# Kernel optimization log

Measured on AMD Instinct MI355X. Metric: run time of the kernel, lower is better.

## Reference

```python
import jax, jax.numpy as jnp
import numpy as np

N, E, D, H, ED, L = 50000, 800000, 256, 8, 16, 6
C = D // H  # 32
NEG_SLOPE = 0.2
EPS = 1e-5


def setup_inputs() -> dict:
    key = jax.random.key(0)
    ks = jax.random.split(key, 16)
    f32 = jnp.float32
    return {
        "x": jax.random.normal(ks[0], (N, D), f32),
        "edge_index": jax.random.randint(ks[1], (2, E), 0, N, dtype=jnp.int64),
        "edge_attr": jax.random.normal(ks[2], (E, ED), f32),
        # shared GATConv params (single conv reused every step, as in the source)
        "W": jax.random.normal(ks[3], (D, D), f32) / np.sqrt(D),
        "att_src": jax.random.normal(ks[4], (H, C), f32) * 0.05,
        "att_dst": jax.random.normal(ks[5], (H, C), f32) * 0.05,
        "att_edge": jax.random.normal(ks[6], (H, C), f32) * 0.05,
        "W_edge": jax.random.normal(ks[7], (ED, D), f32) / np.sqrt(ED),
        "bias": jnp.zeros((D,), f32),
        # per-step FFN + LayerNorm params
        "ffn_w1": jax.random.normal(ks[8], (L, D, 4 * D), f32) / np.sqrt(D),
        "ffn_b1": jnp.zeros((L, 4 * D), f32),
        "ffn_w2": jax.random.normal(ks[9], (L, 4 * D, D), f32) / np.sqrt(4 * D),
        "ffn_b2": jnp.zeros((L, D), f32),
        "ln1_g": jnp.ones((L, D), f32),
        "ln1_b": jnp.zeros((L, D), f32),
        "ln2_g": jnp.ones((L, D), f32),
        "ln2_b": jnp.zeros((L, D), f32),
    }


def _layernorm(x, g, b):
    mu = jnp.mean(x, -1, keepdims=True)
    var = jnp.mean(jnp.square(x - mu), -1, keepdims=True)
    return (x - mu) * jax.lax.rsqrt(var + EPS) * g + b


def _gat_conv(m, edge_index, edge_attr, W, att_src, att_dst, att_edge, W_edge, bias):
    n = m.shape[0]
    x_proj = (m @ W).reshape(n, H, C)  # [N,H,C]
    # add self loops; edge_attr fill_value='mean' (PyG default): mean of incoming edge feats
    src0, dst0 = edge_index[0], edge_index[1]
    deg = jax.ops.segment_sum(jnp.ones_like(dst0, jnp.float32), dst0, n)
    ea_mean = jax.ops.segment_sum(edge_attr, dst0, n) / jnp.maximum(deg, 1.0)[:, None]
    loop = jnp.arange(n, dtype=src0.dtype)
    src = jnp.concatenate([src0, loop])
    dst = jnp.concatenate([dst0, loop])
    ea = jnp.concatenate([edge_attr, ea_mean], 0)
    e_proj = (ea @ W_edge).reshape(-1, H, C)  # [E+N,H,C]
    a_src = jnp.sum(x_proj * att_src, -1)  # [N,H]
    a_dst = jnp.sum(x_proj * att_dst, -1)  # [N,H]
    a_edge = jnp.sum(e_proj * att_edge, -1)  # [E+N,H]
    alpha = jax.nn.leaky_relu(a_src[src] + a_dst[dst] + a_edge, NEG_SLOPE)
    # softmax over edges grouped by destination node
    amax = jax.ops.segment_max(alpha, dst, n)  # every node has a self loop
    ex = jnp.exp(alpha - amax[dst])
    denom = jax.ops.segment_sum(ex, dst, n)
    attn = ex / denom[dst]  # [E+N,H]
    msg = x_proj[src] * attn[:, :, None]  # [E+N,H,C]
    out = jax.ops.segment_sum(msg, dst, n).reshape(n, H * C)
    return out + bias


def reference(x, edge_index, edge_attr, W, att_src, att_dst, att_edge, W_edge, bias,
              ffn_w1, ffn_b1, ffn_w2, ffn_b2, ln1_g, ln1_b, ln2_g, ln2_b):
    m = x
    for i in range(L):
        g = _gat_conv(m, edge_index, edge_attr, W, att_src, att_dst, att_edge, W_edge, bias)
        m = _layernorm(g + m, ln1_g[i], ln1_b[i])  # dropout is identity in eval
        h = jax.nn.relu(m @ ffn_w1[i] + ffn_b1[i]) @ ffn_w2[i] + ffn_b2[i]
        m = _layernorm(h + m, ln2_g[i], ln2_b[i])
    return m
```

## Files before the change

kernel.cpp:

```cpp
#include <hip/hip_runtime.h>
#include <math.h>

#define NN 50000
#define MP 50048
#define EE 800000
#define DD 256
#define HH 8
#define CC 32
#define EDIMK 16
#define LL 6
#define HID 1024
#define NEG 0.2f
#define LNEPS 1e-5f

using short8  = __attribute__((ext_vector_type(8))) short;
using floatx4 = __attribute__((ext_vector_type(4))) float;

static __device__ __forceinline__ float4 ld4(const float* p) {
    return *reinterpret_cast<const float4*>(p);
}
static __device__ __forceinline__ void st4(float* p, float4 v) {
    *reinterpret_cast<float4*>(p) = v;
}
static __device__ __forceinline__ float b2f(unsigned short u) {
    union { unsigned int i; float f; } v; v.i = ((unsigned int)u) << 16; return v.f;
}
static __device__ __forceinline__ unsigned short f2b(float f) {
    union { float f; unsigned int i; } v; v.f = f;
    unsigned int r = (v.i + 0x7fffu + ((v.i >> 16) & 1u)) >> 16;
    return (unsigned short)r;
}
static __device__ __forceinline__ void gload_lds16(const ushort* g, ushort* l) {
    __builtin_amdgcn_global_load_lds((const __attribute__((address_space(1))) void*)g,
                                     (__attribute__((address_space(3))) void*)l, 16, 0, 0);
}

__global__ void k_weh(const float* __restrict__ W_edge, const float* __restrict__ att_edge,
                      float* __restrict__ w_eh) {
    int t = threadIdx.x;
    if (t < EDIMK * HH) {
        int k = t >> 3, h = t & 7;
        float s = 0.f;
        for (int c = 0; c < CC; ++c) s += W_edge[k * DD + h * CC + c] * att_edge[h * CC + c];
        w_eh[t] = s;
    }
}

__global__ void k_edge_pre(const float* __restrict__ edge_attr, const int* __restrict__ ei,
                           const float* __restrict__ w_eh, float* __restrict__ a_edge,
                           int* __restrict__ deg) {
    __shared__ float sw[EDIMK * HH];
    if (threadIdx.x < EDIMK * HH) sw[threadIdx.x] = w_eh[threadIdx.x];
    __syncthreads();
    int e = blockIdx.x * blockDim.x + threadIdx.x;
    if (e >= EE) return;
    float ea[EDIMK];
#pragma unroll
    for (int k4 = 0; k4 < EDIMK; k4 += 4) {
        float4 v = ld4(edge_attr + (size_t)e * EDIMK + k4);
        ea[k4] = v.x; ea[k4 + 1] = v.y; ea[k4 + 2] = v.z; ea[k4 + 3] = v.w;
    }
#pragma unroll
    for (int h = 0; h < HH; ++h) {
        float s = 0.f;
#pragma unroll
        for (int k = 0; k < EDIMK; ++k) s += ea[k] * sw[k * HH + h];
        a_edge[(size_t)e * HH + h] = s;
    }
    atomicAdd(&deg[ei[EE + e]], 1);
}

__global__ void k_scan(const int* __restrict__ deg, int* __restrict__ rowptr) {
    __shared__ int sd[1024];
    __shared__ int soff;
    int tid = threadIdx.x;
    if (tid == 0) { soff = 0; rowptr[0] = 0; }
    __syncthreads();
    for (int base = 0; base < NN; base += 1024) {
        int v = (base + tid < NN) ? deg[base + tid] : 0;
        sd[tid] = v;
        __syncthreads();
        for (int s = 1; s < 1024; s <<= 1) {
            int t2 = (tid >= s) ? sd[tid - s] : 0;
            __syncthreads();
            sd[tid] += t2;
            __syncthreads();
        }
        int incl = sd[tid];
        int off = soff;
        if (base + tid < NN) rowptr[base + tid + 1] = off + incl;
        __syncthreads();
        if (tid == 1023) soff = off + incl;
        __syncthreads();
    }
}

__global__ void k_scatter(const int* __restrict__ ei, const int* __restrict__ rowptr,
                          int* __restrict__ cursor, int* __restrict__ s_src,
                          int* __restrict__ s_eid) {
    int e = blockIdx.x * blockDim.x + threadIdx.x;
    if (e >= EE) return;
    int dst = ei[EE + e];
    int p = rowptr[dst] + atomicAdd(&cursor[dst], 1);
    s_src[p] = ei[e];
    s_eid[p] = e;
}

__global__ void k_permute(const int* __restrict__ s_eid, const float* __restrict__ a_edge,
                          float* __restrict__ ae_csr) {
    size_t t = (size_t)blockIdx.x * blockDim.x + threadIdx.x;
    if (t >= (size_t)EE * HH) return;
    ae_csr[t] = a_edge[(size_t)s_eid[t >> 3] * HH + (t & 7)];
}

__global__ void k_selfmean(const int* __restrict__ rowptr, const float* __restrict__ ae_csr,
                           float* __restrict__ a_self) {
    int t = blockIdx.x * blockDim.x + threadIdx.x;
    if (t >= NN * HH) return;
    int n = t >> 3, h = t & 7;
    int k0 = rowptr[n], k1 = rowptr[n + 1];
    float s = 0.f;
    for (int k = k0; k < k1; ++k) s += ae_csr[(size_t)k * HH + h];
    int d = k1 - k0; if (d < 1) d = 1;
    a_self[t] = s / (float)d;
}

__global__ __launch_bounds__(1024) void k_trans(const float* __restrict__ src,
                                                ushort* __restrict__ dst, int K, int N) {
    __shared__ float s[32][33];
    const float* S = src + (size_t)blockIdx.z * K * N;
    ushort* D = dst + (size_t)blockIdx.z * K * N;
    int n0 = blockIdx.x * 32, k0 = blockIdx.y * 32;
    s[threadIdx.y][threadIdx.x] = S[(size_t)(k0 + threadIdx.y) * N + n0 + threadIdx.x];
    __syncthreads();
    D[(size_t)(n0 + threadIdx.y) * K + k0 + threadIdx.x] = f2b(s[threadIdx.x][threadIdx.y]);
}

__global__ void k_cvt(const float* __restrict__ x, float* __restrict__ m,
                      ushort* __restrict__ mb) {
    int t = blockIdx.x * blockDim.x + threadIdx.x;
    if (t >= NN * DD) return;
    float v = x[t];
    m[t] = v;
    mb[t] = f2b(v);
}

__global__ __launch_bounds__(256) void k_gemm_bf16(const ushort* __restrict__ A,
                                                   const ushort* __restrict__ Bt,
                                                   const float* __restrict__ bias,
                                                   void* __restrict__ Cout,
                                                   int Nc, int K, int mode) {
    __shared__ ushort As[128 * 32];
    __shared__ ushort Bs[128 * 32];
    int tid = threadIdx.x;
    int w = tid >> 6, lane = tid & 63;
    int tileM = blockIdx.y * 128, tileN = blockIdx.x * 128;
    int lrow = lane >> 2, slot = lane & 3;
    int rA0 = w * 16 + lrow, rA1 = (w + 4) * 16 + lrow;
    int cA0 = (slot - (rA0 >> 1)) & 3;
    int cA1 = (slot - (rA1 >> 1)) & 3;
    const ushort* gA0 = A + (size_t)(tileM + rA0) * K + cA0 * 8;
    const ushort* gA1 = A + (size_t)(tileM + rA1) * K + cA1 * 8;
    const ushort* gB0 = Bt + (size_t)(tileN + rA0) * K + cA0 * 8;
    const ushort* gB1 = Bt + (size_t)(tileN + rA1) * K + cA1 * 8;
    ushort* lA0 = As + w * 512;
    ushort* lA1 = As + (w + 4) * 512;
    ushort* lB0 = Bs + w * 512;
    ushort* lB1 = Bs + (w + 4) * 512;
    int wr = w >> 1, wc = w & 1;
    int fr = lane & 15, q = lane >> 4;
    int sf = (q + (fr >> 1)) & 3;
    const ushort* fA = As + (wr * 64 + fr) * 32 + sf * 8;
    const ushort* fB = Bs + (wc * 64 + fr) * 32 + sf * 8;
    floatx4 acc[4][4] = {};
    for (int k0 = 0; k0 < K; k0 += 32) {
        __syncthreads();
        gload_lds16(gA0 + k0, lA0);
        gload_lds16(gA1 + k0, lA1);
        gload_lds16(gB0 + k0, lB0);
        gload_lds16(gB1 + k0, lB1);
        __syncthreads();
        short8 af[4], bf[4];
#pragma unroll
        for (int i = 0; i < 4; ++i) af[i] = *(const short8*)(fA + i * 16 * 32);
#pragma unroll
        for (int j = 0; j < 4; ++j) bf[j] = *(const short8*)(fB + j * 16 * 32);
#pragma unroll
        for (int i = 0; i < 4; ++i)
#pragma unroll
            for (int j = 0; j < 4; ++j)
                acc[i][j] = __builtin_amdgcn_mfma_f32_16x16x32_bf16(af[i], bf[j], acc[i][j], 0, 0, 0);
    }
    int rbase = tileM + wr * 64 + q * 4;
    int cbase = tileN + wc * 64 + fr;
#pragma unroll
    for (int j = 0; j < 4; ++j) {
        int col = cbase + j * 16;
        float bb = (mode != 1) ? bias[col] : 0.f;
#pragma unroll
        for (int i = 0; i < 4; ++i) {
            int row = rbase + i * 16;
#pragma unroll
            for (int r = 0; r < 4; ++r) {
                float v = acc[i][j][r] + bb;
                if (mode == 2 && v < 0.f) v = 0.f;
                if (mode == 0)
                    ((float*)Cout)[(size_t)(row + r) * Nc + col] = v;
                else
                    ((ushort*)Cout)[(size_t)(row + r) * Nc + col] = f2b(v);
            }
        }
    }
}

__global__ void k_srcdst(const ushort* __restrict__ xb, const float* __restrict__ att_src,
                         const float* __restrict__ att_dst, float* __restrict__ a_src,
                         float* __restrict__ a_dst) {
    __shared__ float ss[DD], sd[DD];
    int tid = threadIdx.x;
    if (tid < DD) { ss[tid] = att_src[tid]; sd[tid] = att_dst[tid]; }
    __syncthreads();
    int t = blockIdx.x * blockDim.x + tid;
    if (t >= NN * HH) return;
    int n = t >> 3, h = t & 7;
    const ushort* xp = xb + (size_t)n * DD + h * CC;
    float s1 = 0.f, s2 = 0.f;
#pragma unroll
    for (int c = 0; c < CC; c += 4) {
        ushort4 u = *(const ushort4*)(xp + c);
        float vx = b2f(u.x), vy = b2f(u.y), vz = b2f(u.z), vw = b2f(u.w);
        int b = h * CC + c;
        s1 += vx * ss[b] + vy * ss[b + 1] + vz * ss[b + 2] + vw * ss[b + 3];
        s2 += vx * sd[b] + vy * sd[b + 1] + vz * sd[b + 2] + vw * sd[b + 3];
    }
    a_src[t] = s1;
    a_dst[t] = s2;
}

__global__ __launch_bounds__(256) void k_agg(const ushort* __restrict__ xb,
                                             const float* __restrict__ a_src,
                                             const float* __restrict__ a_dst,
                                             const float* __restrict__ a_self,
                                             const int* __restrict__ rowptr,
                                             const int* __restrict__ s_src,
                                             const float* __restrict__ ae_csr,
                                             const float* __restrict__ bias,
                                             const float* __restrict__ gma,
                                             const float* __restrict__ bta,
                                             float* __restrict__ m,
                                             ushort* __restrict__ mb) {
    int wid = (blockIdx.x * blockDim.x + threadIdx.x) >> 6;
    int lane = threadIdx.x & 63;
    if (wid >= NN) return;
    int n = wid, h = lane >> 3, c4 = lane * 4;
    float adn = a_dst[n * HH + h];
    float al0 = a_src[n * HH + h] + adn + a_self[n * HH + h];
    al0 = al0 > 0.f ? al0 : NEG * al0;
    float w0 = __expf(al0);
    ushort4 xs = *(const ushort4*)(xb + (size_t)n * DD + c4);
    float den = w0;
    float ax = w0 * b2f(xs.x), ay = w0 * b2f(xs.y);
    float az = w0 * b2f(xs.z), aw = w0 * b2f(xs.w);
    int k0 = rowptr[n], k1 = rowptr[n + 1];
    int sNext = (k0 < k1) ? s_src[k0] : 0;
    for (int k = k0; k < k1; ++k) {
        int s = sNext;
        if (k + 1 < k1) sNext = s_src[k + 1];
        float al = a_src[(size_t)s * HH + h] + adn + ae_csr[(size_t)k * HH + h];
        al = al > 0.f ? al : NEG * al;
        float wv = __expf(al);
        den += wv;
        ushort4 v = *(const ushort4*)(xb + (size_t)s * DD + c4);
        ax += wv * b2f(v.x); ay += wv * b2f(v.y);
        az += wv * b2f(v.z); aw += wv * b2f(v.w);
    }
    float inv = 1.f / den;
    size_t base = (size_t)n * DD + c4;
    float4 mr = ld4(m + base);
    float4 b4 = ld4(bias + c4);
    float gx = ax * inv + b4.x + mr.x;
    float gy = ay * inv + b4.y + mr.y;
    float gz = az * inv + b4.z + mr.z;
    float gw = aw * inv + b4.w + mr.w;
    float s = gx + gy + gz + gw;
    for (int off = 32; off; off >>= 1) s += __shfl_xor(s, off, 64);
    float mu = s * (1.0f / DD);
    float dx = gx - mu, dy = gy - mu, dz = gz - mu, dw = gw - mu;
    float qv = dx * dx + dy * dy + dz * dz + dw * dw;
    for (int off = 32; off; off >>= 1) qv += __shfl_xor(qv, off, 64);
    float rs = rsqrtf(qv * (1.0f / DD) + LNEPS);
    float4 g4 = ld4(gma + c4), bb = ld4(bta + c4);
    float4 o;
    o.x = dx * rs * g4.x + bb.x; o.y = dy * rs * g4.y + bb.y;
    o.z = dz * rs * g4.z + bb.z; o.w = dw * rs * g4.w + bb.w;
    st4(m + base, o);
    ushort4 ob;
    ob.x = f2b(o.x); ob.y = f2b(o.y); ob.z = f2b(o.z); ob.w = f2b(o.w);
    *reinterpret_cast<ushort4*>(mb + base) = ob;
}

__global__ __launch_bounds__(256) void k_addln2(const float* __restrict__ a,
                                                const float* __restrict__ gma,
                                                const float* __restrict__ bta,
                                                float* __restrict__ m,
                                                ushort* __restrict__ mb) {
    int wid = (blockIdx.x * blockDim.x + threadIdx.x) >> 6;
    int lane = threadIdx.x & 63;
    if (wid >= NN) return;
    size_t base = (size_t)wid * DD + lane * 4;
    float4 va = ld4(a + base), vb = ld4(m + base);
    float4 v;
    v.x = va.x + vb.x; v.y = va.y + vb.y; v.z = va.z + vb.z; v.w = va.w + vb.w;
    float s = v.x + v.y + v.z + v.w;
    for (int off = 32; off; off >>= 1) s += __shfl_xor(s, off, 64);
    float mu = s * (1.0f / DD);
    float4 d;
    d.x = v.x - mu; d.y = v.y - mu; d.z = v.z - mu; d.w = v.w - mu;
    float qv = d.x * d.x + d.y * d.y + d.z * d.z + d.w * d.w;
    for (int off = 32; off; off >>= 1) qv += __shfl_xor(qv, off, 64);
    float rs = rsqrtf(qv * (1.0f / DD) + LNEPS);
    float4 g4 = ld4(gma + lane * 4), b4 = ld4(bta + lane * 4);
    float4 o;
    o.x = d.x * rs * g4.x + b4.x; o.y = d.y * rs * g4.y + b4.y;
    o.z = d.z * rs * g4.z + b4.z; o.w = d.w * rs * g4.w + b4.w;
    st4(m + base, o);
    ushort4 ob;
    ob.x = f2b(o.x); ob.y = f2b(o.y); ob.z = f2b(o.z); ob.w = f2b(o.w);
    *reinterpret_cast<ushort4*>(mb + base) = ob;
}

extern "C" void kernel_launch(void* const* d_in, const int* in_sizes, int n_in,
                              void* d_out, int out_size, void* d_ws, size_t ws_size,
                              hipStream_t stream) {
    const float* x        = (const float*)d_in[0];
    const int*   ei       = (const int*)d_in[1];
    const float* edge_attr= (const float*)d_in[2];
    const float* W        = (const float*)d_in[3];
    const float* att_src  = (const float*)d_in[4];
    const float* att_dst  = (const float*)d_in[5];
    const float* att_edge = (const float*)d_in[6];
    const float* W_edge   = (const float*)d_in[7];
    const float* bias     = (const float*)d_in[8];
    const float* ffn_w1   = (const float*)d_in[9];
    const float* ffn_b1   = (const float*)d_in[10];
    const float* ffn_w2   = (const float*)d_in[11];
    const float* ffn_b2   = (const float*)d_in[12];
    const float* ln1_g    = (const float*)d_in[13];
    const float* ln1_b    = (const float*)d_in[14];
    const float* ln2_g    = (const float*)d_in[15];
    const float* ln2_b    = (const float*)d_in[16];
    float* m = (float*)d_out;

    char* wp = (char*)d_ws;
    auto alloc = [&](size_t bytes) -> char* {
        char* p = wp;
        wp += (bytes + 255) & ~(size_t)255;
        return p;
    };
    float*  a_edge = (float*)alloc((size_t)EE * HH * 4);
    float*  ae_csr = (float*)alloc((size_t)EE * HH * 4);
    float*  a_self = (float*)alloc((size_t)NN * HH * 4);
    float*  a_src  = (float*)alloc((size_t)NN * HH * 4);
    float*  a_dst  = (float*)alloc((size_t)NN * HH * 4);
    int*    deg    = (int*)alloc((size_t)NN * 4);
    int*    rowptr = (int*)alloc((size_t)(NN + 1) * 4);
    int*    cursor = (int*)alloc((size_t)NN * 4);
    int*    s_src  = (int*)alloc((size_t)EE * 4);
    int*    s_eid  = (int*)alloc((size_t)EE * 4);
    float*  w_eh   = (float*)alloc((size_t)EDIMK * HH * 4);
    ushort* Wt     = (ushort*)alloc((size_t)DD * DD * 2);
    ushort* w1t    = (ushort*)alloc((size_t)LL * DD * HID * 2);
    ushort* w2t    = (ushort*)alloc((size_t)LL * HID * DD * 2);
    ushort* xprojb = (ushort*)alloc((size_t)MP * DD * 2);
    ushort* m_b    = (ushort*)alloc((size_t)MP * DD * 2);
    float*  gbuf   = (float*)alloc((size_t)MP * DD * 4);
    size_t used = (size_t)(wp - (char*)d_ws);
    size_t avail = ws_size > used ? ws_size - used : 0;
    size_t maxrows = avail / ((size_t)HID * 2);
    int chunkP = (int)((maxrows / 128) * 128);
    if (chunkP < 128) chunkP = 128;
    if (chunkP > MP) chunkP = MP;
    ushort* h1b = (ushort*)wp;

    hipMemsetAsync(deg, 0, (size_t)NN * 4, stream);
    hipMemsetAsync(cursor, 0, (size_t)NN * 4, stream);

    k_weh<<<1, 128, 0, stream>>>(W_edge, att_edge, w_eh);
    k_edge_pre<<<(EE + 255) / 256, 256, 0, stream>>>(edge_attr, ei, w_eh, a_edge, deg);
    k_scan<<<1, 1024, 0, stream>>>(deg, rowptr);
    k_scatter<<<(EE + 255) / 256, 256, 0, stream>>>(ei, rowptr, cursor, s_src, s_eid);
    k_permute<<<(EE * HH + 255) / 256, 256, 0, stream>>>(s_eid, a_edge, ae_csr);
    k_selfmean<<<(NN * HH + 255) / 256, 256, 0, stream>>>(rowptr, ae_csr, a_self);
    k_trans<<<dim3(DD / 32, DD / 32, 1), dim3(32, 32), 0, stream>>>(W, Wt, DD, DD);
    k_trans<<<dim3(HID / 32, DD / 32, LL), dim3(32, 32), 0, stream>>>(ffn_w1, w1t, DD, HID);
    k_trans<<<dim3(DD / 32, HID / 32, LL), dim3(32, 32), 0, stream>>>(ffn_w2, w2t, HID, DD);
    k_cvt<<<(NN * DD + 255) / 256, 256, 0, stream>>>(x, m, m_b);

    for (int i = 0; i < LL; ++i) {
        k_gemm_bf16<<<dim3(DD / 128, MP / 128), 256, 0, stream>>>(m_b, Wt, nullptr, xprojb, DD, DD, 1);
        k_srcdst<<<(NN * HH + 255) / 256, 256, 0, stream>>>(xprojb, att_src, att_dst, a_src, a_dst);
        k_agg<<<(NN * 64 + 255) / 256, 256, 0, stream>>>(xprojb, a_src, a_dst, a_self, rowptr,
                                                         s_src, ae_csr, bias,
                                                         ln1_g + i * DD, ln1_b + i * DD, m, m_b);
        for (int r0 = 0; r0 < MP; r0 += chunkP) {
            int rows = (MP - r0) < chunkP ? (MP - r0) : chunkP;
            k_gemm_bf16<<<dim3(HID / 128, rows / 128), 256, 0, stream>>>(
                m_b + (size_t)r0 * DD, w1t + (size_t)i * DD * HID,
                ffn_b1 + (size_t)i * HID, h1b, HID, DD, 2);
            k_gemm_bf16<<<dim3(DD / 128, rows / 128), 256, 0, stream>>>(
                h1b, w2t + (size_t)i * HID * DD,
                ffn_b2 + (size_t)i * DD, gbuf + (size_t)r0 * DD, DD, HID, 0);
        }
        k_addln2<<<(NN * 64 + 255) / 256, 256, 0, stream>>>(gbuf, ln2_g + i * DD, ln2_b + i * DD, m, m_b);
    }
}
```

Baseline: 2.286 ms.

## Deepen GEMM K-tile, widen aggregation, parallelize scan, store FFN output in bf16

Measured after the change: 2.000 ms. 12.5% less time.

```diff
diff --git a/kernel.cpp b/kernel.cpp
--- a/kernel.cpp
+++ b/kernel.cpp
@@ -12,9 +12,11 @@
 #define HID 1024
 #define NEG 0.2f
 #define LNEPS 1e-5f
-
-using short8  = __attribute__((ext_vector_type(8))) short;
-using floatx4 = __attribute__((ext_vector_type(4))) float;
+#define NPARTS ((NN + 255) / 256)
+
+using short8   = __attribute__((ext_vector_type(8))) short;
+using ushort8  = __attribute__((ext_vector_type(8))) unsigned short;
+using floatx4  = __attribute__((ext_vector_type(4))) float;
 
 static __device__ __forceinline__ float4 ld4(const float* p) {
     return *reinterpret_cast<const float4*>(p);
@@ -70,29 +72,49 @@
     atomicAdd(&deg[ei[EE + e]], 1);
 }
 
-__global__ void k_scan(const int* __restrict__ deg, int* __restrict__ rowptr) {
-    __shared__ int sd[1024];
-    __shared__ int soff;
-    int tid = threadIdx.x;
-    if (tid == 0) { soff = 0; rowptr[0] = 0; }
+__global__ __launch_bounds__(256) void k_scan1(const int* __restrict__ deg,
+                                               int* __restrict__ rowptr,
+                                               int* __restrict__ part) {
+    __shared__ int wsum[4];
+    int tid = threadIdx.x, wid = tid >> 6, lane = tid & 63;
+    int g = blockIdx.x * 256 + tid;
+    int v = (g < NN) ? deg[g] : 0;
+    int s = v;
+#pragma unroll
+    for (int off = 1; off < 64; off <<= 1) {
+        int t = __shfl_up(s, off, 64);
+        if (lane >= off) s += t;
+    }
+    if (lane == 63) wsum[wid] = s;
     __syncthreads();
-    for (int base = 0; base < NN; base += 1024) {
-        int v = (base + tid < NN) ? deg[base + tid] : 0;
-        sd[tid] = v;
-        __syncthreads();
-        for (int s = 1; s < 1024; s <<= 1) {
-            int t2 = (tid >= s) ? sd[tid - s] : 0;
-            __syncthreads();
-            sd[tid] += t2;
-            __syncthreads();
-        }
-        int incl = sd[tid];
-        int off = soff;
-        if (base + tid < NN) rowptr[base + tid + 1] = off + incl;
-        __syncthreads();
-        if (tid == 1023) soff = off + incl;
-        __syncthreads();
-    }
+    int woff = 0;
+    for (int i = 0; i < wid; ++i) woff += wsum[i];
+    s += woff;
+    if (g < NN) rowptr[g + 1] = s;
+    if (tid == 255) part[blockIdx.x] = s;
+}
+__global__ __launch_bounds__(256) void k_scan2(int* __restrict__ part) {
+    __shared__ int wsum[4];
+    int tid = threadIdx.x, wid = tid >> 6, lane = tid & 63;
+    int v = (tid < NPARTS) ? part[tid] : 0;
+    int s = v;
+#pragma unroll
+    for (int off = 1; off < 64; off <<= 1) {
+        int t = __shfl_up(s, off, 64);
+        if (lane >= off) s += t;
+    }
+    if (lane == 63) wsum[wid] = s;
+    __syncthreads();
+    int woff = 0;
+    for (int i = 0; i < wid; ++i) woff += wsum[i];
+    s += woff;
+    if (tid < NPARTS) part[tid] = s - v;
+}
+__global__ __launch_bounds__(256) void k_scan3(int* __restrict__ rowptr,
+                                               const int* __restrict__ part) {
+    int g = blockIdx.x * 256 + threadIdx.x;
+    if (g == 0) rowptr[0] = 0;
+    if (g < NN) rowptr[g + 1] += part[blockIdx.x];
 }
 
 __global__ void k_scatter(const int* __restrict__ ei, const int* __restrict__ rowptr,
@@ -150,46 +172,49 @@
                                                    const float* __restrict__ bias,
                                                    void* __restrict__ Cout,
                                                    int Nc, int K, int mode) {
-    __shared__ ushort As[128 * 32];
-    __shared__ ushort Bs[128 * 32];
+    __shared__ ushort As[128 * 64];
+    __shared__ ushort Bs[128 * 64];
     int tid = threadIdx.x;
     int w = tid >> 6, lane = tid & 63;
     int tileM = blockIdx.y * 128, tileN = blockIdx.x * 128;
-    int lrow = lane >> 2, slot = lane & 3;
-    int rA0 = w * 16 + lrow, rA1 = (w + 4) * 16 + lrow;
-    int cA0 = (slot - (rA0 >> 1)) & 3;
-    int cA1 = (slot - (rA1 >> 1)) & 3;
-    const ushort* gA0 = A + (size_t)(tileM + rA0) * K + cA0 * 8;
-    const ushort* gA1 = A + (size_t)(tileM + rA1) * K + cA1 * 8;
-    const ushort* gB0 = Bt + (size_t)(tileN + rA0) * K + cA0 * 8;
-    const ushort* gB1 = Bt + (size_t)(tileN + rA1) * K + cA1 * 8;
-    ushort* lA0 = As + w * 512;
-    ushort* lA1 = As + (w + 4) * 512;
-    ushort* lB0 = Bs + w * 512;
-    ushort* lB1 = Bs + (w + 4) * 512;
+    const ushort* gA[4]; const ushort* gB[4];
+    ushort* lA[4]; ushort* lB[4];
+#pragma unroll
+    for (int p = 0; p < 4; ++p) {
+        int c = (p * 4 + w) * 64 + lane;
+        int row = c >> 3, slot = c & 7;
+        int gs = slot ^ (row & 7);
+        gA[p] = A + (size_t)(tileM + row) * K + gs * 8;
+        gB[p] = Bt + (size_t)(tileN + row) * K + gs * 8;
+        lA[p] = As + (size_t)c * 8;
+        lB[p] = Bs + (size_t)c * 8;
+    }
     int wr = w >> 1, wc = w & 1;
     int fr = lane & 15, q = lane >> 4;
-    int sf = (q + (fr >> 1)) & 3;
-    const ushort* fA = As + (wr * 64 + fr) * 32 + sf * 8;
-    const ushort* fB = Bs + (wc * 64 + fr) * 32 + sf * 8;
     floatx4 acc[4][4] = {};
-    for (int k0 = 0; k0 < K; k0 += 32) {
+    for (int k0 = 0; k0 < K; k0 += 64) {
         __syncthreads();
-        gload_lds16(gA0 + k0, lA0);
-        gload_lds16(gA1 + k0, lA1);
-        gload_lds16(gB0 + k0, lB0);
-        gload_lds16(gB1 + k0, lB1);
+#pragma unroll
+        for (int p = 0; p < 4; ++p) gload_lds16(gA[p] + k0, lA[p]);
+#pragma unroll
+        for (int p = 0; p < 4; ++p) gload_lds16(gB[p] + k0, lB[p]);
         __syncthreads();
-        short8 af[4], bf[4];
-#pragma unroll
-        for (int i = 0; i < 4; ++i) af[i] = *(const short8*)(fA + i * 16 * 32);
-#pragma unroll
-        for (int j = 0; j < 4; ++j) bf[j] = *(const short8*)(fB + j * 16 * 32);
-#pragma unroll
-        for (int i = 0; i < 4; ++i)
+#pragma unroll
+        for (int kc = 0; kc < 2; ++kc) {
+            int ps = ((kc * 4 + q) ^ (fr & 7)) * 8;
+            short8 af[4], bf[4];
+#pragma unroll
+            for (int i = 0; i < 4; ++i)
+                af[i] = *(const short8*)(As + (wr * 64 + i * 16 + fr) * 64 + ps);
 #pragma unroll
             for (int j = 0; j < 4; ++j)
-                acc[i][j] = __builtin_amdgcn_mfma_f32_16x16x32_bf16(af[i], bf[j], acc[i][j], 0, 0, 0);
+                bf[j] = *(const short8*)(Bs + (wc * 64 + j * 16 + fr) * 64 + ps);
+#pragma unroll
+            for (int i = 0; i < 4; ++i)
+#pragma unroll
+                for (int j = 0; j < 4; ++j)
+                    acc[i][j] = __builtin_amdgcn_mfma_f32_16x16x32_bf16(af[i], bf[j], acc[i][j], 0, 0, 0);
+        }
     }
     int rbase = tileM + wr * 64 + q * 4;
     int cbase = tileN + wc * 64 + fr;
@@ -251,55 +276,79 @@
                                              ushort* __restrict__ mb) {
     int wid = (blockIdx.x * blockDim.x + threadIdx.x) >> 6;
     int lane = threadIdx.x & 63;
-    if (wid >= NN) return;
-    int n = wid, h = lane >> 3, c4 = lane * 4;
+    int n = wid * 2 + (lane >> 5);
+    if (n >= NN) return;
+    int hl = lane & 31, h = hl >> 2, c8 = hl * 8;
     float adn = a_dst[n * HH + h];
     float al0 = a_src[n * HH + h] + adn + a_self[n * HH + h];
     al0 = al0 > 0.f ? al0 : NEG * al0;
     float w0 = __expf(al0);
-    ushort4 xs = *(const ushort4*)(xb + (size_t)n * DD + c4);
+    ushort8 xs = *(const ushort8*)(xb + (size_t)n * DD + c8);
+    float acc[8];
+#pragma unroll
+    for (int i = 0; i < 8; ++i) acc[i] = w0 * b2f(xs[i]);
     float den = w0;
-    float ax = w0 * b2f(xs.x), ay = w0 * b2f(xs.y);
-    float az = w0 * b2f(xs.z), aw = w0 * b2f(xs.w);
-    int k0 = rowptr[n], k1 = rowptr[n + 1];
-    int sNext = (k0 < k1) ? s_src[k0] : 0;
-    for (int k = k0; k < k1; ++k) {
-        int s = sNext;
-        if (k + 1 < k1) sNext = s_src[k + 1];
-        float al = a_src[(size_t)s * HH + h] + adn + ae_csr[(size_t)k * HH + h];
-        al = al > 0.f ? al : NEG * al;
-        float wv = __expf(al);
-        den += wv;
-        ushort4 v = *(const ushort4*)(xb + (size_t)s * DD + c4);
-        ax += wv * b2f(v.x); ay += wv * b2f(v.y);
-        az += wv * b2f(v.z); aw += wv * b2f(v.w);
+    int k = rowptr[n], k1 = rowptr[n + 1];
+    for (; k + 1 < k1; k += 2) {
+        int s0 = s_src[k], s1 = s_src[k + 1];
+        float t0 = a_src[(size_t)s0 * HH + h] + adn + ae_csr[(size_t)k * HH + h];
+        float t1 = a_src[(size_t)s1 * HH + h] + adn + ae_csr[(size_t)(k + 1) * HH + h];
+        t0 = t0 > 0.f ? t0 : NEG * t0;
+        t1 = t1 > 0.f ? t1 : NEG * t1;
+        float wv0 = __expf(t0), wv1 = __expf(t1);
+        ushort8 v0 = *(const ushort8*)(xb + (size_t)s0 * DD + c8);
+        ushort8 v1 = *(const ushort8*)(xb + (size_t)s1 * DD + c8);
+        den += wv0 + wv1;
+#pragma unroll
+        for (int i = 0; i < 8; ++i) acc[i] += wv0 * b2f(v0[i]) + wv1 * b2f(v1[i]);
+    }
+    if (k < k1) {
+        int s0 = s_src[k];
+        float t0 = a_src[(size_t)s0 * HH + h] + adn + ae_csr[(size_t)k * HH + h];
+        t0 = t0 > 0.f ? t0 : NEG * t0;
+        float wv0 = __expf(t0);
+        ushort8 v0 = *(const ushort8*)(xb + (size_t)s0 * DD + c8);
+        den += wv0;
+#pragma unroll
+        for (int i = 0; i < 8; ++i) acc[i] += wv0 * b2f(v0[i]);
     }
     float inv = 1.f / den;
-    size_t base = (size_t)n * DD + c4;
-    float4 mr = ld4(m + base);
-    float4 b4 = ld4(bias + c4);
-    float gx = ax * inv + b4.x + mr.x;
-    float gy = ay * inv + b4.y + mr.y;
-    float gz = az * inv + b4.z + mr.z;
-    float gw = aw * inv + b4.w + mr.w;
-    float s = gx + gy + gz + gw;
-    for (int off = 32; off; off >>= 1) s += __shfl_xor(s, off, 64);
+    size_t base = (size_t)n * DD + c8;
+    float4 mr0 = ld4(m + base), mr1 = ld4(m + base + 4);
+    float4 b0 = ld4(bias + c8), b1 = ld4(bias + c8 + 4);
+    float g[8];
+    g[0] = acc[0] * inv + b0.x + mr0.x; g[1] = acc[1] * inv + b0.y + mr0.y;
+    g[2] = acc[2] * inv + b0.z + mr0.z; g[3] = acc[3] * inv + b0.w + mr0.w;
+    g[4] = acc[4] * inv + b1.x + mr1.x; g[5] = acc[5] * inv + b1.y + mr1.y;
+    g[6] = acc[6] * inv + b1.z + mr1.z; g[7] = acc[7] * inv + b1.w + mr1.w;
+    float s = 0.f;
+#pragma unroll
+    for (int i = 0; i < 8; ++i) s += g[i];
+#pragma unroll
+    for (int off = 16; off; off >>= 1) s += __shfl_xor(s, off, 64);
     float mu = s * (1.0f / DD);
-    float dx = gx - mu, dy = gy - mu, dz = gz - mu, dw = gw - mu;
-    float qv = dx * dx + dy * dy + dz * dz + dw * dw;
-    for (int off = 32; off; off >>= 1) qv += __shfl_xor(qv, off, 64);
+    float qv = 0.f;
+#pragma unroll
+    for (int i = 0; i < 8; ++i) { g[i] -= mu; qv += g[i] * g[i]; }
+#pragma unroll
+    for (int off = 16; off; off >>= 1) qv += __shfl_xor(qv, off, 64);
     float rs = rsqrtf(qv * (1.0f / DD) + LNEPS);
-    float4 g4 = ld4(gma + c4), bb = ld4(bta + c4);
-    float4 o;
-    o.x = dx * rs * g4.x + bb.x; o.y = dy * rs * g4.y + bb.y;
-    o.z = dz * rs * g4.z + bb.z; o.w = dw * rs * g4.w + bb.w;
-    st4(m + base, o);
-    ushort4 ob;
-    ob.x = f2b(o.x); ob.y = f2b(o.y); ob.z = f2b(o.z); ob.w = f2b(o.w);
-    *reinterpret_cast<ushort4*>(mb + base) = ob;
-}
-
-__global__ __launch_bounds__(256) void k_addln2(const float* __restrict__ a,
+    float4 g0 = ld4(gma + c8), g1 = ld4(gma + c8 + 4);
+    float4 bb0 = ld4(bta + c8), bb1 = ld4(bta + c8 + 4);
+    float o[8];
+    o[0] = g[0] * rs * g0.x + bb0.x; o[1] = g[1] * rs * g0.y + bb0.y;
+    o[2] = g[2] * rs * g0.z + bb0.z; o[3] = g[3] * rs * g0.w + bb0.w;
+    o[4] = g[4] * rs * g1.x + bb1.x; o[5] = g[5] * rs * g1.y + bb1.y;
+    o[6] = g[6] * rs * g1.z + bb1.z; o[7] = g[7] * rs * g1.w + bb1.w;
+    st4(m + base, make_float4(o[0], o[1], o[2], o[3]));
+    st4(m + base + 4, make_float4(o[4], o[5], o[6], o[7]));
+    ushort8 ob;
+#pragma unroll
+    for (int i = 0; i < 8; ++i) ob[i] = f2b(o[i]);
+    *reinterpret_cast<ushort8*>(mb + base) = ob;
+}
+
+__global__ __launch_bounds__(256) void k_addln2(const ushort* __restrict__ a,
                                                 const float* __restrict__ gma,
                                                 const float* __restrict__ bta,
                                                 float* __restrict__ m,
@@ -308,9 +357,11 @@
     int lane = threadIdx.x & 63;
     if (wid >= NN) return;
     size_t base = (size_t)wid * DD + lane * 4;
-    float4 va = ld4(a + base), vb = ld4(m + base);
+    ushort4 ua = *(const ushort4*)(a + base);
+    float4 vb = ld4(m + base);
     float4 v;
-    v.x = va.x + vb.x; v.y = va.y + vb.y; v.z = va.z + vb.z; v.w = va.w + vb.w;
+    v.x = b2f(ua.x) + vb.x; v.y = b2f(ua.y) + vb.y;
+    v.z = b2f(ua.z) + vb.z; v.w = b2f(ua.w) + vb.w;
     float s = v.x + v.y + v.z + v.w;
     for (int off = 32; off; off >>= 1) s += __shfl_xor(s, off, 64);
     float mu = s * (1.0f / DD);
@@ -365,6 +416,7 @@
     int*    deg    = (int*)alloc((size_t)NN * 4);
     int*    rowptr = (int*)alloc((size_t)(NN + 1) * 4);
     int*    cursor = (int*)alloc((size_t)NN * 4);
+    int*    part   = (int*)alloc((size_t)NPARTS * 4);
     int*    s_src  = (int*)alloc((size_t)EE * 4);
     int*    s_eid  = (int*)alloc((size_t)EE * 4);
     float*  w_eh   = (float*)alloc((size_t)EDIMK * HH * 4);
@@ -373,7 +425,7 @@
     ushort* w2t    = (ushort*)alloc((size_t)LL * HID * DD * 2);
     ushort* xprojb = (ushort*)alloc((size_t)MP * DD * 2);
     ushort* m_b    = (ushort*)alloc((size_t)MP * DD * 2);
-    float*  gbuf   = (float*)alloc((size_t)MP * DD * 4);
+    ushort* gbuf   = (ushort*)alloc((size_t)MP * DD * 2);
     size_t used = (size_t)(wp - (char*)d_ws);
     size_t avail = ws_size > used ? ws_size - used : 0;
     size_t maxrows = avail / ((size_t)HID * 2);
@@ -387,7 +439,9 @@
 
     k_weh<<<1, 128, 0, stream>>>(W_edge, att_edge, w_eh);
     k_edge_pre<<<(EE + 255) / 256, 256, 0, stream>>>(edge_attr, ei, w_eh, a_edge, deg);
-    k_scan<<<1, 1024, 0, stream>>>(deg, rowptr);
+    k_scan1<<<NPARTS, 256, 0, stream>>>(deg, rowptr, part);
+    k_scan2<<<1, 256, 0, stream>>>(part);
+    k_scan3<<<NPARTS, 256, 0, stream>>>(rowptr, part);
     k_scatter<<<(EE + 255) / 256, 256, 0, stream>>>(ei, rowptr, cursor, s_src, s_eid);
     k_permute<<<(EE * HH + 255) / 256, 256, 0, stream>>>(s_eid, a_edge, ae_csr);
     k_selfmean<<<(NN * HH + 255) / 256, 256, 0, stream>>>(rowptr, ae_csr, a_self);
@@ -399,9 +453,9 @@
     for (int i = 0; i < LL; ++i) {
         k_gemm_bf16<<<dim3(DD / 128, MP / 128), 256, 0, stream>>>(m_b, Wt, nullptr, xprojb, DD, DD, 1);
         k_srcdst<<<(NN * HH + 255) / 256, 256, 0, stream>>>(xprojb, att_src, att_dst, a_src, a_dst);
-        k_agg<<<(NN * 64 + 255) / 256, 256, 0, stream>>>(xprojb, a_src, a_dst, a_self, rowptr,
-                                                         s_src, ae_csr, bias,
-                                                         ln1_g + i * DD, ln1_b + i * DD, m, m_b);
+        k_agg<<<((NN + 1) / 2 * 64 + 255) / 256, 256, 0, stream>>>(xprojb, a_src, a_dst, a_self,
+                                                                   rowptr, s_src, ae_csr, bias,
+                                                                   ln1_g + i * DD, ln1_b + i * DD, m, m_b);
         for (int r0 = 0; r0 < MP; r0 += chunkP) {
             int rows = (MP - r0) < chunkP ? (MP - r0) : chunkP;
             k_gemm_bf16<<<dim3(HID / 128, rows / 128), 256, 0, stream>>>(
@@ -409,7 +463,7 @@
                 ffn_b1 + (size_t)i * HID, h1b, HID, DD, 2);
             k_gemm_bf16<<<dim3(DD / 128, rows / 128), 256, 0, stream>>>(
                 h1b, w2t + (size_t)i * HID * DD,
-                ffn_b2 + (size_t)i * DD, gbuf + (size_t)r0 * DD, DD, HID, 0);
+                ffn_b2 + (size_t)i * DD, gbuf + (size_t)r0 * DD, DD, HID, 3);
         }
         k_addln2<<<(NN * 64 + 255) / 256, 256, 0, stream>>>(gbuf, ln2_g + i * DD, ln2_b + i * DD, m, m_b);
     }
```
